# Kernel optimization log

Hardware: AMD Instinct MI355X
Metric: run time of the kernel (lower is better)

## Reference

```python
import jax, jax.numpy as jnp
import numpy as np

D_MODEL = 1024
N_HEADS = 16
D_K = 64  # per-head dim and the scaling denominator used by the module
NEG = -1e9  # stand-in for -inf in masked_fill (rows are never fully masked)


def setup_inputs() -> dict:
    key = jax.random.key(0)
    ks = jax.random.split(key, 8)
    B, M, N = 2, 2048, 2048
    q = jax.random.normal(ks[0], (B, M, D_MODEL), dtype=jnp.float32)
    k = jax.random.normal(ks[1], (B, N, D_MODEL), dtype=jnp.float32)
    v = jax.random.normal(ks[2], (B, N, D_MODEL), dtype=jnp.float32)
    mask = jax.random.randint(ks[3], (B, M, N), 0, 2).astype(jnp.bool_)
    # xavier_uniform for square [d,d] weights: limit = sqrt(6/(d+d))
    lim = float(np.sqrt(6.0 / (D_MODEL + D_MODEL)))
    Wq = jax.random.uniform(ks[4], (D_MODEL, D_MODEL), jnp.float32, -lim, lim)
    Wk = jax.random.uniform(ks[5], (D_MODEL, D_MODEL), jnp.float32, -lim, lim)
    Wv = jax.random.uniform(ks[6], (D_MODEL, D_MODEL), jnp.float32, -lim, lim)
    Wo = jax.random.uniform(ks[7], (D_MODEL, D_MODEL), jnp.float32, -lim, lim)
    return {"q": q, "k": k, "v": v, "mask": mask,
            "Wq": Wq, "Wk": Wk, "Wv": Wv, "Wo": Wo}


def _split_heads(x):
    # (B, S, D) -> (B, H, S, Dh); the torch split/cat-on-batch trick is
    # mathematically identical to this standard head reshape.
    B, S, _ = x.shape
    return x.reshape(B, S, N_HEADS, D_K).transpose(0, 2, 1, 3)


def reference(q, k, v, mask, Wq, Wk, Wv, Wo):
    qw = _split_heads(q @ Wq.T)  # (B,H,M,Dh)
    kw = _split_heads(k @ Wk.T)  # (B,H,N,Dh)
    vw = _split_heads(v @ Wv.T)  # (B,H,N,Dh)
    scores = jnp.einsum('bhmd,bhnd->bhmn', qw, kw)
    scores = jnp.where(mask[:, None, :, :], NEG, scores)
    attn = jax.nn.softmax(scores / jnp.sqrt(jnp.float32(D_K)), axis=-1)
    ctx = jnp.einsum('bhmn,bhnd->bhmd', attn, vw)
    B, _, M, _ = ctx.shape
    ctx = ctx.transpose(0, 2, 1, 3).reshape(B, M, D_MODEL)
    return ctx @ Wo.T
```

## Files before the change

### kernel.cpp

```cpp
#include <hip/hip_runtime.h>
#include <hip/hip_bf16.h>
#include <stdint.h>
#include <string.h>

#define SEQ   2048
#define DM    1024
#define NH    16
#define NB    2

typedef __attribute__((ext_vector_type(8))) short bf16x8;
typedef __attribute__((ext_vector_type(4))) float f32x4;
typedef unsigned short u16;
typedef unsigned int   u32;

__device__ __forceinline__ u16 f2bf(float f) {
    u32 u = __float_as_uint(f);
    u += 0x7FFF + ((u >> 16) & 1);
    return (u16)(u >> 16);
}
__device__ __forceinline__ u32 pk2bf(float a, float b) {
    __hip_bfloat162 p = __float22bfloat162_rn(make_float2(a, b));
    u32 u; memcpy(&u, &p, 4); return u;
}
__device__ __forceinline__ float fexp2(float x) {
#if __has_builtin(__builtin_amdgcn_exp2f)
    return __builtin_amdgcn_exp2f(x);
#else
    return exp2f(x);
#endif
}
__device__ __forceinline__ float mask_exp2(float s, u32 lsel, int pos) {
#if __has_builtin(__builtin_amdgcn_sbfe)
    u32 keep = (u32)__builtin_amdgcn_sbfe((int)lsel, pos, 1);
#else
    u32 keep = (u32)((int)(lsel << (31 - pos)) >> 31);
#endif
    return __uint_as_float(__float_as_uint(fexp2(s)) & keep);
}
__device__ __forceinline__ void gl_lds16(const void* g, void* l) {
    __builtin_amdgcn_global_load_lds(
        (const __attribute__((address_space(1))) u32*)g,
        (__attribute__((address_space(3))) u32*)l, 16, 0, 0);
}
__device__ __forceinline__ void wbar_vm2() { asm volatile("s_waitcnt vmcnt(2)\ns_barrier" ::: "memory"); }
__device__ __forceinline__ void wbar_vm3() { asm volatile("s_waitcnt vmcnt(3)\ns_barrier" ::: "memory"); }
__device__ __forceinline__ void wbar_vm4() { asm volatile("s_waitcnt vmcnt(4)\ns_barrier" ::: "memory"); }
__device__ __forceinline__ void bar()      { asm volatile("s_barrier" ::: "memory"); }
__device__ __forceinline__ void vm_drain() { asm volatile("s_waitcnt vmcnt(0)" ::: "memory"); }

struct CvtArgs {
    const float* s[7];
    u16* d[7];
    float scale[7];
    int start[8];
    const int* mask;
    u32* mbits;
};
__global__ __launch_bounds__(256) void cvt_kernel(CvtArgs a) {
    int bid = blockIdx.x;
    int tid = threadIdx.x;
    if (bid >= 8192) {
        int widx = (bid - 8192) * 256 + tid;
        uint4 v = ((const uint4*)a.mask)[widx];
        unsigned long long b0 = __ballot(v.x != 0);
        unsigned long long b1 = __ballot(v.y != 0);
        unsigned long long b2 = __ballot(v.z != 0);
        unsigned long long b3 = __ballot(v.w != 0);
        int lane = tid & 63;
        if (lane < 4) {
            int sh = lane * 16;
            u32 lo = (u32)((b0 >> sh) & 0xFFFF) | ((u32)((b1 >> sh) & 0xFFFF) << 16);
            u32 hi = (u32)((b2 >> sh) & 0xFFFF) | ((u32)((b3 >> sh) & 0xFFFF) << 16);
            size_t N = (size_t)(bid - 8192) * 1024 + (size_t)(tid >> 6) * 256
                     + (size_t)lane * 64;
            u32* dst = a.mbits + ((N >> 11) * 64 + ((N >> 6) & 31) * 2);
            *(uint2*)dst = make_uint2(lo, hi);
        }
        return;
    }
    int seg = 0;
#pragma unroll
    for (int i = 1; i < 7; ++i) if (bid >= a.start[i]) seg = i;
    float sc = a.scale[seg];
    size_t base = (size_t)(bid - a.start[seg]) * 2048 + tid * 8;
    const float4* s4 = (const float4*)(a.s[seg] + base);
    float4 x = s4[0], y = s4[1];
    u32 r[4];
    r[0] = pk2bf(x.x*sc, x.y*sc); r[1] = pk2bf(x.z*sc, x.w*sc);
    r[2] = pk2bf(y.x*sc, y.y*sc); r[3] = pk2bf(y.z*sc, y.w*sc);
    *(uint4*)(a.d[seg] + base) = *(uint4*)r;
}

template<int RT>
__device__ __forceinline__ void gemm_body(const u16* __restrict__ A,
                                          const u16* __restrict__ Bm,
                                          void* __restrict__ Y,
                                          int rtile, int ctile, int mode,
                                          u16* sA, u16* sB) {
    constexpr int ABUF = RT * 32 * 32;
    constexpr int BBUF = 128 * 32;
    const int tid  = threadIdx.x;
    const int wv   = tid >> 6, lane = tid & 63;
    const int quad = lane >> 4, ln = lane & 15;
    const int wr   = wv >> 1,  wc  = wv & 1;

    const int lr4 = lane >> 2;
    const int lcc = ((lane & 3) ^ ((lane >> 3) & 3)) * 8;

    const u16* gA[RT/2]; u16* lA[RT/2];
#pragma unroll
    for (int s = 0; s < RT/2; ++s) {
        int seg = wv * (RT/2) + s;
        gA[s] = A + (size_t)(rtile * (RT*32) + seg*16 + lr4) * 1024 + lcc;
        lA[s] = sA + seg * 512;
    }
    const u16* gB[2]; u16* lB[2];
#pragma unroll
    for (int s = 0; s < 2; ++s) {
        int seg = wv * 2 + s;
        gB[s] = Bm + (size_t)(ctile * 128 + seg*16 + lr4) * 1024 + lcc;
        lB[s] = sB + seg * 512;
    }

    f32x4 acc[RT][4];
#pragma unroll
    for (int i = 0; i < RT; ++i)
#pragma unroll
        for (int j = 0; j < 4; ++j) acc[i][j] = (f32x4){0.f,0.f,0.f,0.f};

    const int c0 = (quad ^ ((ln >> 1) & 3)) * 8;

#pragma unroll
    for (int s = 0; s < RT/2; ++s) gl_lds16(gA[s], lA[s]);
#pragma unroll
    for (int s = 0; s < 2; ++s)    gl_lds16(gB[s], lB[s]);
#pragma unroll
    for (int s = 0; s < RT/2; ++s) gl_lds16(gA[s] + 32, lA[s] + ABUF);
#pragma unroll
    for (int s = 0; s < 2; ++s)    gl_lds16(gB[s] + 32, lB[s] + BBUF);

    int bc = 0, bp = 2;
    for (int kt = 0; kt < 32; ++kt) {
        if (RT == 4) wbar_vm4(); else wbar_vm3();
        int pk = (kt + 2) & 31;
#pragma unroll
        for (int s = 0; s < RT/2; ++s) gl_lds16(gA[s] + pk*32, lA[s] + bp*ABUF);
#pragma unroll
        for (int s = 0; s < 2; ++s)    gl_lds16(gB[s] + pk*32, lB[s] + bp*BBUF);

        const u16* sAb = sA + bc * ABUF;
        const u16* sBb = sB + bc * BBUF;
        bf16x8 af[RT], bfr[4];
#pragma unroll
        for (int rt = 0; rt < RT; ++rt)
            af[rt] = *(const bf16x8*)(sAb + (wr*(RT*16) + rt*16 + ln) * 32 + c0);
#pragma unroll
        for (int ct = 0; ct < 4; ++ct)
            bfr[ct] = *(const bf16x8*)(sBb + (wc*64 + ct*16 + ln) * 32 + c0);
#pragma unroll
        for (int rt = 0; rt < RT; ++rt)
#pragma unroll
            for (int ct = 0; ct < 4; ++ct)
                acc[rt][ct] = __builtin_amdgcn_mfma_f32_16x16x32_bf16(
                    af[rt], bfr[ct], acc[rt][ct], 0, 0, 0);

        bc = (bc == 2) ? 0 : bc + 1;
        bp = (bp == 2) ? 0 : bp + 1;
    }
    vm_drain();

#pragma unroll
    for (int rt = 0; rt < RT; ++rt) {
#pragma unroll
        for (int ct = 0; ct < 4; ++ct) {
#pragma unroll
            for (int i = 0; i < 4; ++i) {
                int R = rtile*(RT*32) + wr*(RT*16) + rt*16 + quad*4 + i;
                int C = ctile*128 + wc*64 + ct*16 + ln;
                float val = acc[rt][ct][i];
                if (mode == 0) {
                    int b = R >> 11, s = R & 2047, h = C >> 6, d = C & 63;
                    ((u16*)Y)[((size_t)((b*NH + h) * SEQ + s) << 6) + d] = f2bf(val);
                } else if (mode == 1) {
                    int h = R >> 6, d = R & 63, b = C >> 11, n = C & 2047;
                    int nl = n & 63;
                    int np = (nl & 32) | (((nl & 15) >> 2) << 3) | (nl & 3)
                           | ((nl & 16) >> 2);
                    n = (n & ~63) | np;
                    ((u16*)Y)[((size_t)((b*NH + h) * 64 + d) << 11) + n] = f2bf(val);
                } else {
                    ((float*)Y)[(size_t)R * 1024 + C] = val;
                }
            }
        }
    }
}

struct QKVArgs { const u16* A[3]; const u16* B[3]; u16* Y[3]; };

__global__ __launch_bounds__(512, 2) void gemm_qkv256(QKVArgs g) {
    __shared__ __align__(16) u16 smem[65536];

    const int z  = blockIdx.y;
    const int bx = blockIdx.x;
    int rtile, ctile, mode;
    if (z == 2) { rtile = bx & 3;  ctile = bx >> 2; mode = 1; }
    else        { rtile = bx >> 2; ctile = bx & 3;  mode = 0; }
    const u16* Aa = g.A[z];
    const u16* Ba = g.B[z];
    u16*       Yy = g.Y[z];

    const int tid  = threadIdx.x;
    const int wv   = tid >> 6, lane = tid & 63;
    const int quad = lane >> 4, ln = lane & 15;
    const int wr   = wv >> 2,  wc  = wv & 3;

    const int r0  = tid >> 3;
    const int lcq = ((tid & 7) ^ (r0 & 7)) * 8;
    const u16* srcs[4];
    srcs[0] = Aa + (size_t)(rtile*256 +       r0) * 1024 + lcq;
    srcs[1] = Aa + (size_t)(rtile*256 + 128 + r0) * 1024 + lcq;
    srcs[2] = Ba + (size_t)(ctile*256 +       r0) * 1024 + lcq;
    srcs[3] = Ba + (size_t)(ctile*256 + 128 + r0) * 1024 + lcq;

    const int sw3 = (ln & 7) << 3;
    const int cs0 = (quad * 8) ^ sw3;
    const int cs1 = (32 + quad * 8) ^ sw3;
    const u16* aA  = smem + wr*8192 + ln*64 + cs0;
    const u16* aA2 = smem + wr*8192 + ln*64 + cs1;
    const u16* bB  = smem + 16384 + (wc>>1)*8192 + (wc&1)*4096 + ln*64 + cs0;
    const u16* bB2 = smem + 16384 + (wc>>1)*8192 + (wc&1)*4096 + ln*64 + cs1;

    f32x4 acc[8][4];
#pragma unroll
    for (int i = 0; i < 8; ++i)
#pragma unroll
        for (int j = 0; j < 4; ++j) acc[i][j] = (f32x4){0.f,0.f,0.f,0.f};

#pragma unroll
    for (int p = 0; p < 4; ++p) {
        u16* dst = smem + p*8192 + wv*512;
        gl_lds16(srcs[p], dst);
        gl_lds16(srcs[p] + 65536, dst + 4096);
    }

    for (int kt = 0; kt < 16; ++kt) {
        const int D  = (kt & 1) << 15;
        const int Dp = D ^ 32768;
        const int pk = (kt + 1) & 15;
        bf16x8 af[8][2];
#pragma unroll
        for (int p = 0; p < 4; ++p) {
            u16* dst = smem + Dp + p*8192 + wv*512;
            gl_lds16(srcs[p] + pk*64, dst);
            gl_lds16(srcs[p] + pk*64 + 65536, dst + 4096);
            if (p == 0) wbar_vm2(); else bar();
            if (p == 0) {
#pragma unroll
                for (int mf = 0; mf < 8; ++mf) {
                    af[mf][0] = *(const bf16x8*)(aA  + D + mf*1024);
                    af[mf][1] = *(const bf16x8*)(aA2 + D + mf*1024);
                }
            }
            bf16x8 b0 = *(const bf16x8*)(bB  + D + p*1024);
            bf16x8 b1 = *(const bf16x8*)(bB2 + D + p*1024);
            __builtin_amdgcn_s_setprio(1);
#pragma unroll
            for (int mf = 0; mf < 8; ++mf) {
                acc[mf][p] = __builtin_amdgcn_mfma_f32_16x16x32_bf16(
                    af[mf][0], b0, acc[mf][p], 0, 0, 0);
                acc[mf][p] = __builtin_amdgcn_mfma_f32_16x16x32_bf16(
                    af[mf][1], b1, acc[mf][p], 0, 0, 0);
            }
            __builtin_amdgcn_s_setprio(0);
        }
    }
    vm_drain();

#pragma unroll
    for (int mf = 0; mf < 8; ++mf)
#pragma unroll
        for (int nf = 0; nf < 4; ++nf)
#pragma unroll
            for (int i = 0; i < 4; ++i) {
                int R = rtile*256 + wr*128 + mf*16 + quad*4 + i;
                int C = ctile*256 + wc*64 + nf*16 + ln;
                float val = acc[mf][nf][i];
                if (mode == 0) {
                    int b = R >> 11, s = R & 2047, h = C >> 6, d = C & 63;
                    Yy[((size_t)((b*NH + h) * SEQ + s) << 6) + d] = f2bf(val);
                } else {
                    int h = R >> 6, d = R & 63, b = C >> 11, n = C & 2047;
                    int nl = n & 63;
                    int np = (nl & 32) | (((nl & 15) >> 2) << 3) | (nl & 3)
                           | ((nl & 16) >> 2);
                    n = (n & ~63) | np;
                    Yy[((size_t)((b*NH + h) * 64 + d) << 11) + n] = f2bf(val);
                }
            }
}

__global__ __launch_bounds__(256) void gemm_out(const u16* __restrict__ A,
                                                const u16* __restrict__ Bm,
                                                float* __restrict__ Y) {
    __shared__ u16 sA[3 * 64 * 32];
    __shared__ u16 sB[3 * 128 * 32];
    gemm_body<2>(A, Bm, Y, blockIdx.x, blockIdx.y, 2, sA, sB);
}

__global__ __launch_bounds__(512, 4) void attn_kernel(
    const u16* __restrict__ qw,
    const u16* __restrict__ kw,
    const u16* __restrict__ vt,
    const u32* __restrict__ mbits,
    u16* __restrict__ ctx) {

    __shared__ __align__(16) u16 smem[32768];
    u16* sK = smem;
    u16* sV = smem + 16384;

    const int mtile = blockIdx.x;
    const int bh    = blockIdx.y;
    const int b     = bh >> 4;
    const int tid   = threadIdx.x;
    const int wv    = tid >> 6, lane = tid & 63;
    const int quad  = lane >> 4, ln = lane & 15;
    const int g     = wv >> 2;
    const int w2    = wv & 3;
    const int m0    = mtile * 128;

    const size_t hbase = (size_t)bh * SEQ * 64;

    bf16x8 qf[2][2];
#pragma unroll
    for (int mt = 0; mt < 2; ++mt) {
        const u16* qp = qw + hbase + (size_t)(m0 + w2*32 + mt*16 + ln) * 64 + quad*8;
        qf[mt][0] = *(const bf16x8*)(qp);
        qf[mt][1] = *(const bf16x8*)(qp + 32);
    }

    f32x4 o[2][4], lsum[2];
#pragma unroll
    for (int mt = 0; mt < 2; ++mt) {
        lsum[mt] = (f32x4){0.f,0.f,0.f,0.f};
#pragma unroll
        for (int j = 0; j < 4; ++j) o[mt][j] = (f32x4){0.f,0.f,0.f,0.f};
    }

    bf16x8 ones;
#pragma unroll
    for (int i = 0; i < 8; ++i) ones[i] = (short)0x3F80;

    const u32* mrow0 = mbits + (size_t)(b*SEQ + m0 + w2*32 + ln) * 64;
    const u32* mrow1 = mrow0 + ((size_t)16 * 64);

    const int lr = lane >> 3;
    const int lc = (lane & 7) ^ lr;
    const u16* gK = kw + hbase + (size_t)(wv*8 + lr) * 64 + lc*8;
    const u16* gV = vt + hbase + (size_t)(wv*8 + lr) * SEQ + lc*8;
    u16* lK = sK + wv * 512;
    u16* lV = sV + wv * 512;

    const int c0 = (quad ^ (ln & 7)) * 8;
    const u16* a1 = smem + ln*64 + c0;
    const u16* a2 = smem + ln*64 + (c0 ^ 32);
    const u16* aK1 = a1 + g*2048;
    const u16* aK2 = a2 + g*2048;
    const u16* aV  = (g ? a2 : a1) + 16384;
    const int  msh = g*8 + quad;

    gl_lds16(gK, lK);
    gl_lds16(gV, lV);
    uint2 wA0 = *(const uint2*)(mrow0);
    uint2 wA1 = *(const uint2*)(mrow1);
    gl_lds16(gK + 4096, lK + 4096);
    gl_lds16(gV + 64,   lV + 4096);
    uint2 wB0 = *(const uint2*)(mrow0 + 2);
    uint2 wB1 = *(const uint2*)(mrow1 + 2);

    for (int mi = 0; mi < 8; ++mi) {
#pragma unroll
        for (int u = 0; u < 4; ++u) {
            const int bc = u;
            const int wb = (u + 2) & 3;
            wbar_vm4();
            int pidx = (mi*4 + u + 2) & 31;
            gl_lds16(gK + (size_t)pidx * 4096, lK + wb*4096);
            gl_lds16(gV + pidx * 64,           lV + wb*4096);
            uint2 wC0 = *(const uint2*)(mrow0 + pidx*2);
            uint2 wC1 = *(const uint2*)(mrow1 + pidx*2);

            f32x4 s4[2][2];
            __builtin_amdgcn_s_setprio(1);
#pragma unroll
            for (int ct2 = 0; ct2 < 2; ++ct2) {
                bf16x8 k0 = *(const bf16x8*)(aK1 + bc*4096 + ct2*1024);
                bf16x8 k1 = *(const bf16x8*)(aK2 + bc*4096 + ct2*1024);
#pragma unroll
                for (int mt = 0; mt < 2; ++mt) {
                    f32x4 zz = (f32x4){0.f, 0.f, 0.f, 0.f};
                    zz = __builtin_amdgcn_mfma_f32_16x16x32_bf16(k0, qf[mt][0], zz, 0, 0, 0);
                    zz = __builtin_amdgcn_mfma_f32_16x16x32_bf16(k1, qf[mt][1], zz, 0, 0, 0);
                    s4[mt][ct2] = zz;
                }
            }
            __builtin_amdgcn_s_setprio(0);

            bf16x8 pfm[2];
#pragma unroll
            for (int mt = 0; mt < 2; ++mt) {
                u32 wx = mt ? wA1.x : wA0.x;
                u32 wy = mt ? wA1.y : wA0.y;
                u32 l0 = ~(wx >> msh);
                u32 l1 = ~(wy >> msh);
                u32 P[4];
#pragma unroll
                for (int ct2 = 0; ct2 < 2; ++ct2) {
                    float p[4];
                    p[0] = mask_exp2(s4[mt][ct2][0], l0, ct2*4);
                    p[1] = mask_exp2(s4[mt][ct2][1], l0, 16 + ct2*4);
                    p[2] = mask_exp2(s4[mt][ct2][2], l1, ct2*4);
                    p[3] = mask_exp2(s4[mt][ct2][3], l1, 16 + ct2*4);
                    P[ct2*2]     = pk2bf(p[0], p[1]);
                    P[ct2*2 + 1] = pk2bf(p[2], p[3]);
                }
                memcpy(&pfm[mt], P, 16);
            }

            __builtin_amdgcn_s_setprio(1);
            lsum[0] = __builtin_amdgcn_mfma_f32_16x16x32_bf16(pfm[0], ones, lsum[0], 0, 0, 0);
            lsum[1] = __builtin_amdgcn_mfma_f32_16x16x32_bf16(pfm[1], ones, lsum[1], 0, 0, 0);
#pragma unroll
            for (int ct = 0; ct < 4; ++ct) {
                bf16x8 vf = *(const bf16x8*)(aV + bc*4096 + ct*1024);
                o[0][ct] = __builtin_amdgcn_mfma_f32_16x16x32_bf16(pfm[0], vf, o[0][ct], 0, 0, 0);
                o[1][ct] = __builtin_amdgcn_mfma_f32_16x16x32_bf16(pfm[1], vf, o[1][ct], 0, 0, 0);
            }
            __builtin_amdgcn_s_setprio(0);

            wA0 = wB0; wA1 = wB1;
            wB0 = wC0; wB1 = wC1;
        }
    }
    vm_drain();
    __syncthreads();

    float* sO  = (float*)smem;
    float* sLs = (float*)((char*)smem + 34816);
    if (g == 1) {
#pragma unroll
        for (int mt = 0; mt < 2; ++mt)
#pragma unroll
            for (int i = 0; i < 4; ++i) {
                int lm = w2*32 + mt*16 + quad*4 + i;
                sLs[lm] = lsum[mt][i];
#pragma unroll
                for (int ct = 0; ct < 4; ++ct)
                    sO[lm*68 + ct*16 + ln] = o[mt][ct][i];
            }
    }
    __syncthreads();
    if (g == 0) {
#pragma unroll
        for (int mt = 0; mt < 2; ++mt)
#pragma unroll
            for (int i = 0; i < 4; ++i) {
                int lm = w2*32 + mt*16 + quad*4 + i;
                float inv = 1.f / (lsum[mt][i] + sLs[lm]);
                int m = m0 + lm;
                size_t base = ((size_t)(b * SEQ + m) << 10) + (bh & 15) * 64;
#pragma unroll
                for (int ct = 0; ct < 4; ++ct)
                    ctx[base + ct*16 + ln] =
                        f2bf((o[mt][ct][i] + sO[lm*68 + ct*16 + ln]) * inv);
            }
    }
}

extern "C" void kernel_launch(void* const* d_in, const int* in_sizes, int n_in,
                              void* d_out, int out_size, void* d_ws, size_t ws_size,
                              hipStream_t stream) {
    const float* q    = (const float*)d_in[0];
    const float* k    = (const float*)d_in[1];
    const float* v    = (const float*)d_in[2];
    const int*   mask = (const int*)d_in[3];
    const float* Wq   = (const float*)d_in[4];
    const float* Wk   = (const float*)d_in[5];
    const float* Wv   = (const float*)d_in[6];
    const float* Wo   = (const float*)d_in[7];
    float* out = (float*)d_out;

    char* ws = (char*)d_ws;
    const size_t SZH = (size_t)NB * SEQ * DM * 2;
    const size_t SZW = (size_t)DM * DM * 2;
    u16* qw   = (u16*)(ws);
    u16* kw   = (u16*)(ws + SZH);
    u16* vt   = (u16*)(ws + 2*SZH);
    u16* ctx  = (u16*)(ws + 3*SZH);
    u16* vb   = ctx;
    u32* mbits= (u32*)(ws + 4*SZH);
    u16* qb   = (u16*)(ws + 4*SZH + (1u<<20));
    u16* kb   = (u16*)(ws + 4*SZH + (1u<<20) + SZH);
    u16* Wqb  = (u16*)(ws + 4*SZH + (1u<<20) + 2*SZH);
    u16* Wkb  = (u16*)((char*)Wqb + SZW);
    u16* Wvb  = (u16*)((char*)Wqb + 2*SZW);
    u16* Wob  = (u16*)((char*)Wqb + 3*SZW);

    const float CSC = 0.18033688011112042f;

    CvtArgs ca;
    ca.s[0]=q;  ca.d[0]=qb;  ca.scale[0]=1.f;
    ca.s[1]=k;  ca.d[1]=kb;  ca.scale[1]=1.f;
    ca.s[2]=v;  ca.d[2]=vb;  ca.scale[2]=1.f;
    ca.s[3]=Wq; ca.d[3]=Wqb; ca.scale[3]=CSC;
    ca.s[4]=Wk; ca.d[4]=Wkb; ca.scale[4]=1.f;
    ca.s[5]=Wv; ca.d[5]=Wvb; ca.scale[5]=1.f;
    ca.s[6]=Wo; ca.d[6]=Wob; ca.scale[6]=1.f;
    int st[8] = {0, 2048, 4096, 6144, 6656, 7168, 7680, 8192};
    for (int i = 0; i < 8; ++i) ca.start[i] = st[i];
    ca.mask  = mask;
    ca.mbits = mbits;
    cvt_kernel<<<dim3(16384), dim3(256), 0, stream>>>(ca);

    QKVArgs ga;
    ga.A[0]=qb;  ga.B[0]=Wqb; ga.Y[0]=qw;
    ga.A[1]=kb;  ga.B[1]=Wkb; ga.Y[1]=kw;
    ga.A[2]=Wvb; ga.B[2]=vb;  ga.Y[2]=vt;
    gemm_qkv256<<<dim3(64, 3), dim3(512), 0, stream>>>(ga);

    attn_kernel<<<dim3(SEQ/128, NB*NH), dim3(512), 0, stream>>>(qw, kw, vt, mbits, ctx);

    gemm_out<<<dim3(64, 8), dim3(256), 0, stream>>>(ctx, Wob, out);
}
```

Before: 245.5 us.

## Rewrite output projection GEMM with 128x256 tiles, 512 threads, double-buffered BK=64

Replaces the generic 64x128-tile, 256-thread output GEMM with a dedicated kernel using 128x256 tiles, 8 waves, K-step 64 and double buffering. Global-to-LDS loads use an XOR swizzle, are interleaved with the MFMA phases, and MFMA sections run at raised s_setprio. The aim is more data reuse per LDS load and fewer pipeline barriers per K. The cost is a grid of only 128 blocks, which may underfill the GPU's compute units.

```diff
diff --git a/kernel.cpp b/kernel.cpp
--- a/kernel.cpp
+++ b/kernel.cpp
@@ -43,7 +43,6 @@
         (__attribute__((address_space(3))) u32*)l, 16, 0, 0);
 }
 __device__ __forceinline__ void wbar_vm2() { asm volatile("s_waitcnt vmcnt(2)\ns_barrier" ::: "memory"); }
-__device__ __forceinline__ void wbar_vm3() { asm volatile("s_waitcnt vmcnt(3)\ns_barrier" ::: "memory"); }
 __device__ __forceinline__ void wbar_vm4() { asm volatile("s_waitcnt vmcnt(4)\ns_barrier" ::: "memory"); }
 __device__ __forceinline__ void bar()      { asm volatile("s_barrier" ::: "memory"); }
 __device__ __forceinline__ void vm_drain() { asm volatile("s_waitcnt vmcnt(0)" ::: "memory"); }
@@ -91,111 +90,6 @@
     *(uint4*)(a.d[seg] + base) = *(uint4*)r;
 }
 
-template<int RT>
-__device__ __forceinline__ void gemm_body(const u16* __restrict__ A,
-                                          const u16* __restrict__ Bm,
-                                          void* __restrict__ Y,
-                                          int rtile, int ctile, int mode,
-                                          u16* sA, u16* sB) {
-    constexpr int ABUF = RT * 32 * 32;
-    constexpr int BBUF = 128 * 32;
-    const int tid  = threadIdx.x;
-    const int wv   = tid >> 6, lane = tid & 63;
-    const int quad = lane >> 4, ln = lane & 15;
-    const int wr   = wv >> 1,  wc  = wv & 1;
-
-    const int lr4 = lane >> 2;
-    const int lcc = ((lane & 3) ^ ((lane >> 3) & 3)) * 8;
-
-    const u16* gA[RT/2]; u16* lA[RT/2];
-#pragma unroll
-    for (int s = 0; s < RT/2; ++s) {
-        int seg = wv * (RT/2) + s;
-        gA[s] = A + (size_t)(rtile * (RT*32) + seg*16 + lr4) * 1024 + lcc;
-        lA[s] = sA + seg * 512;
-    }
-    const u16* gB[2]; u16* lB[2];
-#pragma unroll
-    for (int s = 0; s < 2; ++s) {
-        int seg = wv * 2 + s;
-        gB[s] = Bm + (size_t)(ctile * 128 + seg*16 + lr4) * 1024 + lcc;
-        lB[s] = sB + seg * 512;
-    }
-
-    f32x4 acc[RT][4];
-#pragma unroll
-    for (int i = 0; i < RT; ++i)
-#pragma unroll
-        for (int j = 0; j < 4; ++j) acc[i][j] = (f32x4){0.f,0.f,0.f,0.f};
-
-    const int c0 = (quad ^ ((ln >> 1) & 3)) * 8;
-
-#pragma unroll
-    for (int s = 0; s < RT/2; ++s) gl_lds16(gA[s], lA[s]);
-#pragma unroll
-    for (int s = 0; s < 2; ++s)    gl_lds16(gB[s], lB[s]);
-#pragma unroll
-    for (int s = 0; s < RT/2; ++s) gl_lds16(gA[s] + 32, lA[s] + ABUF);
-#pragma unroll
-    for (int s = 0; s < 2; ++s)    gl_lds16(gB[s] + 32, lB[s] + BBUF);
-
-    int bc = 0, bp = 2;
-    for (int kt = 0; kt < 32; ++kt) {
-        if (RT == 4) wbar_vm4(); else wbar_vm3();
-        int pk = (kt + 2) & 31;
-#pragma unroll
-        for (int s = 0; s < RT/2; ++s) gl_lds16(gA[s] + pk*32, lA[s] + bp*ABUF);
-#pragma unroll
-        for (int s = 0; s < 2; ++s)    gl_lds16(gB[s] + pk*32, lB[s] + bp*BBUF);
-
-        const u16* sAb = sA + bc * ABUF;
-        const u16* sBb = sB + bc * BBUF;
-        bf16x8 af[RT], bfr[4];
-#pragma unroll
-        for (int rt = 0; rt < RT; ++rt)
-            af[rt] = *(const bf16x8*)(sAb + (wr*(RT*16) + rt*16 + ln) * 32 + c0);
-#pragma unroll
-        for (int ct = 0; ct < 4; ++ct)
-            bfr[ct] = *(const bf16x8*)(sBb + (wc*64 + ct*16 + ln) * 32 + c0);
-#pragma unroll
-        for (int rt = 0; rt < RT; ++rt)
-#pragma unroll
-            for (int ct = 0; ct < 4; ++ct)
-                acc[rt][ct] = __builtin_amdgcn_mfma_f32_16x16x32_bf16(
-                    af[rt], bfr[ct], acc[rt][ct], 0, 0, 0);
-
-        bc = (bc == 2) ? 0 : bc + 1;
-        bp = (bp == 2) ? 0 : bp + 1;
-    }
-    vm_drain();
-
-#pragma unroll
-    for (int rt = 0; rt < RT; ++rt) {
-#pragma unroll
-        for (int ct = 0; ct < 4; ++ct) {
-#pragma unroll
-            for (int i = 0; i < 4; ++i) {
-                int R = rtile*(RT*32) + wr*(RT*16) + rt*16 + quad*4 + i;
-                int C = ctile*128 + wc*64 + ct*16 + ln;
-                float val = acc[rt][ct][i];
-                if (mode == 0) {
-                    int b = R >> 11, s = R & 2047, h = C >> 6, d = C & 63;
-                    ((u16*)Y)[((size_t)((b*NH + h) * SEQ + s) << 6) + d] = f2bf(val);
-                } else if (mode == 1) {
-                    int h = R >> 6, d = R & 63, b = C >> 11, n = C & 2047;
-                    int nl = n & 63;
-                    int np = (nl & 32) | (((nl & 15) >> 2) << 3) | (nl & 3)
-                           | ((nl & 16) >> 2);
-                    n = (n & ~63) | np;
-                    ((u16*)Y)[((size_t)((b*NH + h) * 64 + d) << 11) + n] = f2bf(val);
-                } else {
-                    ((float*)Y)[(size_t)R * 1024 + C] = val;
-                }
-            }
-        }
-    }
-}
-
 struct QKVArgs { const u16* A[3]; const u16* B[3]; u16* Y[3]; };
 
 __global__ __launch_bounds__(512, 2) void gemm_qkv256(QKVArgs g) {
@@ -300,12 +194,92 @@
             }
 }
 
-__global__ __launch_bounds__(256) void gemm_out(const u16* __restrict__ A,
-                                                const u16* __restrict__ Bm,
-                                                float* __restrict__ Y) {
-    __shared__ u16 sA[3 * 64 * 32];
-    __shared__ u16 sB[3 * 128 * 32];
-    gemm_body<2>(A, Bm, Y, blockIdx.x, blockIdx.y, 2, sA, sB);
+__global__ __launch_bounds__(512, 2) void gemm_out256(const u16* __restrict__ A,
+                                                      const u16* __restrict__ Bm,
+                                                      float* __restrict__ Y) {
+    __shared__ __align__(16) u16 smem[49152];
+
+    const int bx = blockIdx.x;
+    const int rtile = bx >> 2, ctile = bx & 3;
+
+    const int tid  = threadIdx.x;
+    const int wv   = tid >> 6, lane = tid & 63;
+    const int quad = lane >> 4, ln = lane & 15;
+    const int wr   = wv >> 2,  wc  = wv & 3;
+
+    const int r0  = tid >> 3;
+    const int lcq = ((tid & 7) ^ (r0 & 7)) * 8;
+    const u16* srcs[3];
+    srcs[0] = A  + (size_t)(rtile*128 +       r0) * 1024 + lcq;
+    srcs[1] = Bm + (size_t)(ctile*256 +       r0) * 1024 + lcq;
+    srcs[2] = Bm + (size_t)(ctile*256 + 128 + r0) * 1024 + lcq;
+
+    const int sw3 = (ln & 7) << 3;
+    const int cs0 = (quad * 8) ^ sw3;
+    const int cs1 = (32 + quad * 8) ^ sw3;
+    const u16* aA  = smem + (wr*64 + ln)*64 + cs0;
+    const u16* aA2 = smem + (wr*64 + ln)*64 + cs1;
+    const u16* bB  = smem + 8192 + (wc*64 + ln)*64 + cs0;
+    const u16* bB2 = smem + 8192 + (wc*64 + ln)*64 + cs1;
+
+    f32x4 acc[4][4];
+#pragma unroll
+    for (int i = 0; i < 4; ++i)
+#pragma unroll
+        for (int j = 0; j < 4; ++j) acc[i][j] = (f32x4){0.f,0.f,0.f,0.f};
+
+#pragma unroll
+    for (int p = 0; p < 3; ++p) {
+        u16* dst = smem + p*8192 + wv*512;
+        gl_lds16(srcs[p], dst);
+        gl_lds16(srcs[p] + 65536, dst + 4096);
+    }
+
+    for (int kt = 0; kt < 16; ++kt) {
+        const int D  = (kt & 1) * 24576;
+        const int Dp = 24576 - D;
+        const int pk = (kt + 1) & 15;
+        bf16x8 af[4][2];
+#pragma unroll
+        for (int p = 0; p < 4; ++p) {
+            if (p < 3) {
+                u16* dst = smem + Dp + p*8192 + wv*512;
+                gl_lds16(srcs[p] + pk*64, dst);
+                gl_lds16(srcs[p] + pk*64 + 65536, dst + 4096);
+            }
+            if (p == 0) wbar_vm2(); else bar();
+            if (p == 0) {
+#pragma unroll
+                for (int mf = 0; mf < 4; ++mf) {
+                    af[mf][0] = *(const bf16x8*)(aA  + D + mf*1024);
+                    af[mf][1] = *(const bf16x8*)(aA2 + D + mf*1024);
+                }
+            }
+            bf16x8 b0 = *(const bf16x8*)(bB  + D + p*1024);
+            bf16x8 b1 = *(const bf16x8*)(bB2 + D + p*1024);
+            __builtin_amdgcn_s_setprio(1);
+#pragma unroll
+            for (int mf = 0; mf < 4; ++mf) {
+                acc[mf][p] = __builtin_amdgcn_mfma_f32_16x16x32_bf16(
+                    af[mf][0], b0, acc[mf][p], 0, 0, 0);
+                acc[mf][p] = __builtin_amdgcn_mfma_f32_16x16x32_bf16(
+                    af[mf][1], b1, acc[mf][p], 0, 0, 0);
+            }
+            __builtin_amdgcn_s_setprio(0);
+        }
+    }
+    vm_drain();
+
+#pragma unroll
+    for (int mf = 0; mf < 4; ++mf)
+#pragma unroll
+        for (int nf = 0; nf < 4; ++nf)
+#pragma unroll
+            for (int i = 0; i < 4; ++i) {
+                int R = rtile*128 + wr*64 + mf*16 + quad*4 + i;
+                int C = ctile*256 + wc*64 + nf*16 + ln;
+                Y[(size_t)R * 1024 + C] = acc[mf][nf][i];
+            }
 }
 
 __global__ __launch_bounds__(512, 4) void attn_kernel(
@@ -530,5 +504,5 @@
 
     attn_kernel<<<dim3(SEQ/128, NB*NH), dim3(512), 0, stream>>>(qw, kw, vt, mbits, ctx);
 
-    gemm_out<<<dim3(64, 8), dim3(256), 0, stream>>>(ctx, Wob, out);
-}
+    gemm_out256<<<dim3(128), dim3(512), 0, stream>>>(ctx, Wob, out);
+}
```

After: 240.6 us. 2.0% less time.
